# Optimization experiments

Hardware: AMD Instinct MI355X
Metric: run time of the kernel (lower is better)

The kernel has to match this reference:

```python
import math
import jax, jax.numpy as jnp
import numpy as np

B, T, C_IN, C_OUT, H, M = 16, 4096, 128, 64, 8, 30
TAU = 1.0
EPS = 1e-6


def _make_projection(m, d, seed=0):
    # FAVOR+ projection: stacked rows of transposed QR orthogonal blocks,
    # scaled by norms of gaussian rows (scaling=0 in the torch source).
    rng = np.random.RandomState(seed)
    blocks = []
    rows = 0
    while rows < m:
        q, _ = np.linalg.qr(rng.randn(d, d))
        blocks.append(q.T)
        rows += d
    final = np.vstack(blocks)[:m]
    multiplier = np.linalg.norm(rng.randn(m, d), axis=1)
    return jnp.asarray((multiplier[:, None] * final).astype(np.float32))


def _kernel_transform(data, proj, is_query):
    # softmax_kernel_transformation from the torch source
    d = data.shape[-1]
    data = data * (float(d) ** -0.25)
    ratio = 1.0 / math.sqrt(proj.shape[0])
    dd = jnp.einsum('bnhd,md->bnhm', data, proj)      # [B,T,H,M]
    diag = jnp.sum(data * data, axis=-1, keepdims=True) / 2.0
    if is_query:
        mx = jnp.max(dd, axis=-1, keepdims=True)
    else:
        mx = jnp.max(dd, axis=(1, 3), keepdims=True)  # max over features and seq
    return ratio * (jnp.exp(dd - diag - mx) + EPS)


def setup_inputs() -> dict:
    key = jax.random.key(0)
    ks = jax.random.split(key, 8)
    s_in = 1.0 / math.sqrt(C_IN)
    s_hid = 1.0 / math.sqrt(C_OUT * H)
    return {
        'x': jax.random.normal(ks[0], (B, T, C_IN), jnp.float32),
        'wq_w': jax.random.uniform(ks[1], (C_OUT * H, C_IN), jnp.float32, -s_in, s_in),
        'wq_b': jnp.zeros((C_OUT * H,), jnp.float32),
        'wk_w': jax.random.uniform(ks[2], (C_OUT * H, C_IN), jnp.float32, -s_in, s_in),
        'wk_b': jnp.zeros((C_OUT * H,), jnp.float32),
        'wv_w': jax.random.uniform(ks[3], (C_OUT * H, C_IN), jnp.float32, -s_in, s_in),
        'wv_b': jnp.zeros((C_OUT * H,), jnp.float32),
        'wo_w': jax.random.uniform(ks[4], (C_OUT, C_OUT * H), jnp.float32, -s_hid, s_hid),
        'wo_b': jnp.zeros((C_OUT,), jnp.float32),
        'proj': _make_projection(M, C_OUT, seed=0),
    }


def reference(x, wq_w, wq_b, wk_w, wk_b, wv_w, wv_b, wo_w, wo_b, proj):
    b, t, _ = x.shape
    inv_sqrt_tau = 1.0 / math.sqrt(TAU)
    q = (x @ wq_w.T + wq_b).reshape(b, t, H, C_OUT) * inv_sqrt_tau
    k = (x @ wk_w.T + wk_b).reshape(b, t, H, C_OUT) * inv_sqrt_tau
    v = (x @ wv_w.T + wv_b).reshape(b, t, H, C_OUT)
    q = _kernel_transform(q, proj, True)   # [B,T,H,M]
    k = _kernel_transform(k, proj, False)  # [B,T,H,M]
    # linear attention: O(T) kv state accumulation
    kvs = jnp.einsum('bnhm,bnhd->bhmd', k, v)
    num = jnp.einsum('bnhm,bhmd->bnhd', q, kvs)
    den = jnp.einsum('bnhm,bhm->bnh', q, jnp.sum(k, axis=1))
    out = num / den[..., None]             # [B,T,H,D]
    return out.reshape(b, t, H * C_OUT) @ wo_w.T + wo_b
```

## Files before the change

kernel.cpp:

```cpp
#include <hip/hip_runtime.h>
#include <cstdint>

typedef __attribute__((ext_vector_type(4))) float f32x4;
typedef __attribute__((ext_vector_type(8))) short short8;
typedef __attribute__((ext_vector_type(8))) unsigned short us8;

#define DEV __device__ __forceinline__

DEV unsigned short f2b(float f) {
  unsigned u = __builtin_bit_cast(unsigned, f);
  return (unsigned short)((u + 0x7fffu + ((u >> 16) & 1u)) >> 16);
}
DEV float b2f(unsigned short h) {
  unsigned u = ((unsigned)h) << 16;
  return __builtin_bit_cast(float, u);
}

constexpr float SQ_SCALE = 0.35355339059327379f;
constexpr float RATIO    = 0.18257418583505536f;
constexpr float REPS     = 0.18257418583505536e-6f;

constexpr size_t OF_WQKV  = 0;
constexpr size_t OF_WBP   = 262144;
constexpr size_t OF_XBF   = 270336;
constexpr size_t OF_XBFT  = 17047552;
constexpr size_t OF_PHIKT = 33824768;
constexpr size_t OF_S2    = 67379200;
constexpr size_t OF_KSUM  = 84156416;
constexpr size_t OF_GT    = 84172800;
constexpr size_t WS_NEED  = 84697088;

__global__ __launch_bounds__(256) void k_prep(
    const float* __restrict__ x, const float* __restrict__ wq,
    const float* __restrict__ wk, const float* __restrict__ bq,
    const float* __restrict__ bk, const float* __restrict__ proj,
    unsigned short* __restrict__ xbf, unsigned short* __restrict__ xbfT,
    unsigned short* __restrict__ wqkv, float* __restrict__ wbp) {
  int tid = threadIdx.x;
  if (blockIdx.x < 1024) {
    __shared__ unsigned short xt[128 * 72];
    int n0 = blockIdx.x * 64;
    int tok = tid & 63, cgrp = tid >> 6;
    const float* src = x + (size_t)(n0 + tok) * 128 + cgrp * 32;
    unsigned short* dst = xbf + (size_t)(n0 + tok) * 128 + cgrp * 32;
#pragma unroll
    for (int q8 = 0; q8 < 4; ++q8) {
      f32x4 a = *reinterpret_cast<const f32x4*>(src + q8 * 8);
      f32x4 c4 = *reinterpret_cast<const f32x4*>(src + q8 * 8 + 4);
      us8 o;
      o[0] = f2b(a[0]); o[1] = f2b(a[1]); o[2] = f2b(a[2]); o[3] = f2b(a[3]);
      o[4] = f2b(c4[0]); o[5] = f2b(c4[1]); o[6] = f2b(c4[2]); o[7] = f2b(c4[3]);
      *reinterpret_cast<us8*>(dst + q8 * 8) = o;
#pragma unroll
      for (int e = 0; e < 8; ++e) {
        int c = cgrp * 32 + q8 * 8 + e;
        *reinterpret_cast<unsigned short*>(((char*)xt) + c * 144 + tok * 2) = o[e];
      }
    }
    __syncthreads();
    int c2 = tid >> 1, half = tid & 1;
    size_t tbase = (size_t)blockIdx.x * 8192;
#pragma unroll
    for (int i = 0; i < 4; ++i) {
      us8 o = *reinterpret_cast<const us8*>(((const char*)xt) + c2 * 144 + half * 64 + i * 16);
      *reinterpret_cast<us8*>(xbfT + tbase + (size_t)tid * 32 + i * 8) = o;
    }
    return;
  }
  int bid = blockIdx.x - 1024;
  if (bid < 256) {
    int id = bid * 256 + tid;
    wqkv[id] = f2b(wk[id] * SQ_SCALE);
  } else if (bid < 272) {
    __shared__ float wsm[64 * 128];
    __shared__ float ps[32 * 64];
    __shared__ float bs[64];
    int db = bid - 256, mat2 = db >> 3, h = db & 7;
    const float* wsrc = (mat2 == 0) ? wq : wk;
    const float* bsrc = (mat2 == 0) ? bq : bk;
    for (int i = tid; i < 8192; i += 256) wsm[i] = wsrc[h * 8192 + i] * SQ_SCALE;
    for (int i = tid; i < 2048; i += 256) {
      int m = i >> 6, d = i & 63;
      ps[i] = (m < 30) ? proj[m * 64 + d] : 0.0f;
    }
    if (tid < 64) bs[tid] = bsrc[h * 64 + tid] * SQ_SCALE;
    __syncthreads();
    int m = tid >> 3, kseg = tid & 7;
    int col = 512 + mat2 * 256 + h * 32 + m;
#pragma unroll 4
    for (int kk = 0; kk < 16; ++kk) {
      int k = kseg * 16 + kk;
      float a = 0.f;
      for (int d = 0; d < 64; ++d) a += ps[m * 64 + d] * wsm[d * 128 + k];
      wqkv[col * 128 + k] = f2b(a);
    }
    if (tid < 32) {
      float a = 0.f;
      for (int d = 0; d < 64; ++d) a += ps[tid * 64 + d] * bs[d];
      wbp[512 + mat2 * 256 + h * 32 + tid] = a;
    }
  } else {
    for (int i = tid; i < 512; i += 256) wbp[i] = bk[i] * SQ_SCALE;
  }
}

DEV void stage_x(const unsigned short* xbf, unsigned short* xs, int n0, int tid) {
  int row = tid >> 2, seg = tid & 3;
  const unsigned short* src = xbf + (size_t)(n0 + row) * 128 + seg * 32;
#pragma unroll
  for (int q8 = 0; q8 < 4; ++q8) {
    us8 o = *reinterpret_cast<const us8*>(src + q8 * 8);
    int byte = (row * 256 + seg * 64 + q8 * 16) ^ ((row & 7) << 4);
    *reinterpret_cast<us8*>(((char*)xs) + byte) = o;
  }
}

__global__ __launch_bounds__(256) void k_qkv(
    const unsigned short* __restrict__ xbf, const unsigned short* __restrict__ wqkv,
    const float* __restrict__ wbp, unsigned short* __restrict__ phikT) {
  __shared__ unsigned short xs[64 * 128];
  __shared__ unsigned short scratch[4][2304];
  __shared__ float diag_s[512];

  int tid = threadIdx.x;
  int w = tid >> 6, l = tid & 63;
  int g = l >> 4, li = l & 15;
  int n0 = blockIdx.x * 64;

  stage_x(xbf, xs, n0, tid);
  __syncthreads();

  const short* wq_s = reinterpret_cast<const short*>(wqkv);
  char* scr = (char*)scratch[w];

  for (int j = 0; j < 3; ++j) {
    if (j == 2) __syncthreads();
    int bcol = (j < 2) ? (j * 256 + w * 64) : (768 + w * 64);

    f32x4 acc[4][4] = {};
#pragma unroll
    for (int ks = 0; ks < 4; ++ks) {
      short8 a[4], bb[4];
#pragma unroll
      for (int fi = 0; fi < 4; ++fi) {
        int tokl = fi * 16 + li;
        int byte = (tokl * 256 + (ks * 32 + g * 8) * 2) ^ ((tokl & 7) << 4);
        a[fi] = *reinterpret_cast<const short8*>(((const char*)xs) + byte);
      }
#pragma unroll
      for (int fj = 0; fj < 4; ++fj)
        bb[fj] = *reinterpret_cast<const short8*>(wq_s + (bcol + fj * 16 + li) * 128 + ks * 32 + g * 8);
#pragma unroll
      for (int fi = 0; fi < 4; ++fi)
#pragma unroll
        for (int fj = 0; fj < 4; ++fj)
          acc[fi][fj] = __builtin_amdgcn_mfma_f32_16x16x32_bf16(a[fi], bb[fj], acc[fi][fj], 0, 0, 0);
    }
#pragma unroll
    for (int fj = 0; fj < 4; ++fj) {
      float bias = wbp[bcol + fj * 16 + li];
#pragma unroll
      for (int fi = 0; fi < 4; ++fi)
#pragma unroll
        for (int r = 0; r < 4; ++r) acc[fi][fj][r] += bias;
    }

    if (j < 2) {
      int h = j * 4 + w;
      float t4[4][4];
#pragma unroll
      for (int fi = 0; fi < 4; ++fi)
#pragma unroll
        for (int r = 0; r < 4; ++r) {
          float s = 0.f;
#pragma unroll
          for (int fj = 0; fj < 4; ++fj) { float v = acc[fi][fj][r]; s += v * v; }
          t4[fi][r] = s;
        }
#pragma unroll
      for (int mask = 1; mask <= 8; mask <<= 1)
#pragma unroll
        for (int fi = 0; fi < 4; ++fi)
#pragma unroll
          for (int r = 0; r < 4; ++r)
            t4[fi][r] += __shfl_xor(t4[fi][r], mask, 64);
      if (li == 0) {
#pragma unroll
        for (int fi = 0; fi < 4; ++fi)
#pragma unroll
          for (int r = 0; r < 4; ++r)
            diag_s[h * 64 + fi * 16 + g * 4 + r] = 0.5f * t4[fi][r];
      }
    } else {
#pragma unroll
      for (int hp = 0; hp < 2; ++hp) {
        int h = w * 2 + hp;
#pragma unroll
        for (int fj2 = 0; fj2 < 2; ++fj2) {
          int m = fj2 * 16 + li;
          bool valid = (m < 30);
#pragma unroll
          for (int fi = 0; fi < 4; ++fi)
#pragma unroll
            for (int r = 0; r < 4; ++r) {
              int tok = fi * 16 + g * 4 + r;
              float ph = valid
                  ? (RATIO * __expf(acc[fi][hp * 2 + fj2][r] - diag_s[h * 64 + tok]) + REPS)
                  : 0.0f;
              *reinterpret_cast<unsigned short*>(scr + m * 144 + tok * 2) = f2b(ph);
            }
        }
        size_t gbase = (size_t)(h * 1024 + blockIdx.x) * 2048;
#pragma unroll
        for (int i = 0; i < 4; ++i) {
          us8 o = *reinterpret_cast<const us8*>(scr + (l >> 1) * 144 + (l & 1) * 64 + i * 16);
          *reinterpret_cast<us8*>(&phikT[gbase + (size_t)l * 32 + i * 8]) = o;
        }
      }
    }
  }
}

__global__ __launch_bounds__(256) void k_S(
    const unsigned short* __restrict__ phikT, const unsigned short* __restrict__ xbfT,
    float* __restrict__ S2, float* __restrict__ ksum) {
  int tid = threadIdx.x;
  int w = tid >> 6, l = tid & 63, g = l >> 4, li = l & 15;
  int bid = blockIdx.x;
  int bh = bid >> 3, chunk = bid & 7;
  int b = bh >> 3, h = bh & 7;
  int tb = b * 64 + chunk * 8;

  const short* pk = reinterpret_cast<const short*>(phikT);
  const short* xt = reinterpret_cast<const short*>(xbfT);

  float s0 = 0.f, s1 = 0.f;
  f32x4 acc[2][2] = {};
#pragma unroll 2
  for (int tile = 0; tile < 8; ++tile) {
    size_t abase = (size_t)(h * 1024 + tb + tile) * 2048;
    size_t bbase = (size_t)(tb + tile) * 8192 + (size_t)(w * 32) * 64;
#pragma unroll
    for (int ks = 0; ks < 2; ++ks) {
      int t = ks * 32 + g * 8;
      short8 a0 = *reinterpret_cast<const short8*>(pk + abase + li * 64 + t);
      short8 a1 = *reinterpret_cast<const short8*>(pk + abase + (16 + li) * 64 + t);
#pragma unroll
      for (int e = 0; e < 8; ++e) {
        s0 += b2f((unsigned short)a0[e]);
        s1 += b2f((unsigned short)a1[e]);
      }
      short8 b0 = *reinterpret_cast<const short8*>(xt + bbase + li * 64 + t);
      short8 b1 = *reinterpret_cast<const short8*>(xt + bbase + (16 + li) * 64 + t);
      acc[0][0] = __builtin_amdgcn_mfma_f32_16x16x32_bf16(a0, b0, acc[0][0], 0, 0, 0);
      acc[1][0] = __builtin_amdgcn_mfma_f32_16x16x32_bf16(a1, b0, acc[1][0], 0, 0, 0);
      acc[0][1] = __builtin_amdgcn_mfma_f32_16x16x32_bf16(a0, b1, acc[0][1], 0, 0, 0);
      acc[1][1] = __builtin_amdgcn_mfma_f32_16x16x32_bf16(a1, b1, acc[1][1], 0, 0, 0);
    }
  }
#pragma unroll
  for (int fm = 0; fm < 2; ++fm)
#pragma unroll
    for (int fc = 0; fc < 2; ++fc)
#pragma unroll
      for (int r = 0; r < 4; ++r) {
        int m = fm * 16 + g * 4 + r;
        int c = w * 32 + fc * 16 + li;
        S2[(size_t)bid * 4096 + m * 128 + c] = acc[fm][fc][r];
      }
  s0 += __shfl_xor(s0, 16, 64); s0 += __shfl_xor(s0, 32, 64);
  s1 += __shfl_xor(s1, 16, 64); s1 += __shfl_xor(s1, 32, 64);
  if (w == 0 && l < 16) {
    atomicAdd(&ksum[bh * 32 + l], s0);
    atomicAdd(&ksum[bh * 32 + 16 + l], s1);
  }
}

__global__ __launch_bounds__(256) void k_fold(
    const float* __restrict__ S2, const float* __restrict__ wv,
    const float* __restrict__ bv, const float* __restrict__ wo,
    const float* __restrict__ ksum, unsigned short* __restrict__ Gt) {
  __shared__ float ss[32 * 128];
  __shared__ float wvs[64 * 128];
  __shared__ float kvl[32 * 64];
  __shared__ float wos[64 * 64];
  __shared__ float bvs[64];
  __shared__ float kss[32];
  int tid = threadIdx.x;
  int bh = blockIdx.x, h = bh & 7;
  for (int i = tid; i < 4096; i += 256) {
    float a = 0.f;
#pragma unroll
    for (int c = 0; c < 8; ++c) a += S2[(size_t)(bh * 8 + c) * 4096 + i];
    ss[i] = a;
  }
  for (int i = tid; i < 8192; i += 256) wvs[i] = wv[(size_t)h * 8192 + i];
  {
    int c = tid >> 2, dseg = tid & 3;
#pragma unroll
    for (int jj = 0; jj < 16; ++jj) {
      int d = dseg * 16 + jj;
      wos[d * 64 + c] = wo[c * 512 + h * 64 + d];
    }
  }
  if (tid < 64) bvs[tid] = bv[h * 64 + tid];
  if (tid < 32) kss[tid] = ksum[bh * 32 + tid];
  __syncthreads();
  {
    int m = tid >> 3, dg = tid & 7;
#pragma unroll
    for (int i = 0; i < 8; ++i) {
      int d = dg * 8 + i;
      float a = kss[m] * bvs[d];
      for (int c = 0; c < 128; ++c) a += ss[m * 128 + c] * wvs[d * 128 + c];
      kvl[m * 64 + d] = a;
    }
  }
  __syncthreads();
  int cp = tid & 63, mseg = tid >> 6;
  us8 outv;
#pragma unroll
  for (int jj = 0; jj < 8; ++jj) {
    int m = mseg * 8 + jj;
    float a = 0.f;
    for (int d = 0; d < 64; ++d) a += kvl[m * 64 + d] * wos[d * 64 + cp];
    outv[jj] = f2b(a);
  }
  *reinterpret_cast<us8*>(Gt + ((size_t)bh * 64 + cp) * 32 + mseg * 8) = outv;
}

__global__ __launch_bounds__(256) void k_out(
    const unsigned short* __restrict__ xbf, const unsigned short* __restrict__ wqkv,
    const float* __restrict__ wbp, const unsigned short* __restrict__ Gt,
    const float* __restrict__ ksum, const float* __restrict__ wob,
    float* __restrict__ out) {
  __shared__ unsigned short phiqs[8 * 2048];

  int tid = threadIdx.x;
  int w = tid >> 6, l = tid & 63;
  int g = l >> 4, li = l & 15;
  int n0 = blockIdx.x * 64;
  int b = n0 >> 12;

  unsigned short* xs = phiqs;
  stage_x(xbf, xs, n0, tid);
  __syncthreads();

  const short* wq_s = reinterpret_cast<const short*>(wqkv);

  int bcol = 512 + w * 64;
  f32x4 acc[4][4] = {};
#pragma unroll
  for (int ks = 0; ks < 4; ++ks) {
    short8 a[4], bb[4];
#pragma unroll
    for (int fi = 0; fi < 4; ++fi) {
      int tokl = fi * 16 + li;
      int byte = (tokl * 256 + (ks * 32 + g * 8) * 2) ^ ((tokl & 7) << 4);
      a[fi] = *reinterpret_cast<const short8*>(((const char*)xs) + byte);
    }
#pragma unroll
    for (int fj = 0; fj < 4; ++fj)
      bb[fj] = *reinterpret_cast<const short8*>(wq_s + (bcol + fj * 16 + li) * 128 + ks * 32 + g * 8);
#pragma unroll
    for (int fi = 0; fi < 4; ++fi)
#pragma unroll
      for (int fj = 0; fj < 4; ++fj)
        acc[fi][fj] = __builtin_amdgcn_mfma_f32_16x16x32_bf16(a[fi], bb[fj], acc[fi][fj], 0, 0, 0);
  }
#pragma unroll
  for (int fj = 0; fj < 4; ++fj) {
    float bias = wbp[bcol + fj * 16 + li];
#pragma unroll
    for (int fi = 0; fi < 4; ++fi)
#pragma unroll
      for (int r = 0; r < 4; ++r) acc[fi][fj][r] += bias;
  }
  __syncthreads();

#pragma unroll
  for (int hp = 0; hp < 2; ++hp) {
    int h = w * 2 + hp;
    char* st = ((char*)phiqs) + h * 4096;
#pragma unroll
    for (int fj2 = 0; fj2 < 2; ++fj2) {
      int m = fj2 * 16 + li;
      bool valid = (m < 30);
#pragma unroll
      for (int fi = 0; fi < 4; ++fi)
#pragma unroll
        for (int r = 0; r < 4; ++r) {
          int tok = fi * 16 + g * 4 + r;
          float ph = valid ? __expf(acc[fi][hp * 2 + fj2][r]) : 0.0f;
          int byte = (tok * 64 + m * 2) ^ ((tok & 7) << 4);
          *reinterpret_cast<unsigned short*>(st + byte) = f2b(ph);
        }
    }
  }
  __syncthreads();

  const short* gt_s = reinterpret_cast<const short*>(Gt);
  int tokl = w * 16 + li;
  f32x4 oacc[4] = {};
#pragma unroll
  for (int h = 0; h < 8; ++h) {
    int bh = b * 8 + h;
    int abyte = h * 4096 + ((tokl * 64 + g * 16) ^ ((tokl & 7) << 4));
    short8 a = *reinterpret_cast<const short8*>(((const char*)phiqs) + abyte);
    const float* ksrow = ksum + bh * 32 + g * 8;
    float den = 0.f;
#pragma unroll
    for (int jj = 0; jj < 8; ++jj) den += b2f((unsigned short)a[jj]) * ksrow[jj];
    den += __shfl_xor(den, 16, 64);
    den += __shfl_xor(den, 32, 64);
    float rd = 1.0f / den;
    f32x4 nm[4];
#pragma unroll
    for (int fj = 0; fj < 4; ++fj) {
      short8 bb = *reinterpret_cast<const short8*>(gt_s + ((size_t)bh * 64 + fj * 16 + li) * 32 + g * 8);
      f32x4 z = {};
      nm[fj] = __builtin_amdgcn_mfma_f32_16x16x32_bf16(a, bb, z, 0, 0, 0);
    }
#pragma unroll
    for (int r = 0; r < 4; ++r) {
      float rdr = __shfl(rd, g * 4 + r, 64);
#pragma unroll
      for (int fj = 0; fj < 4; ++fj) oacc[fj][r] += nm[fj][r] * rdr;
    }
  }
#pragma unroll
  for (int fj = 0; fj < 4; ++fj) {
    float bias = wob[fj * 16 + li];
#pragma unroll
    for (int r = 0; r < 4; ++r) {
      int n = n0 + w * 16 + g * 4 + r;
      out[(size_t)n * 64 + fj * 16 + li] = oacc[fj][r] + bias;
    }
  }
}

extern "C" void kernel_launch(void* const* d_in, const int* in_sizes, int n_in,
                              void* d_out, int out_size, void* d_ws, size_t ws_size,
                              hipStream_t stream) {
  const int expect[10] = {8388608, 65536, 512, 65536, 512, 65536, 512, 32768, 64, 1920};
  if (n_in != 10) return;
  for (int i = 0; i < 10; ++i) if (in_sizes[i] != expect[i]) return;
  if (out_size != 4194304) return;
  if (ws_size < WS_NEED) return;

  const float* x    = (const float*)d_in[0];
  const float* wq   = (const float*)d_in[1];
  const float* bq   = (const float*)d_in[2];
  const float* wk   = (const float*)d_in[3];
  const float* bk   = (const float*)d_in[4];
  const float* wv   = (const float*)d_in[5];
  const float* bv   = (const float*)d_in[6];
  const float* wo   = (const float*)d_in[7];
  const float* wob  = (const float*)d_in[8];
  const float* proj = (const float*)d_in[9];

  char* ws = (char*)d_ws;
  unsigned short* wqkv  = (unsigned short*)(ws + OF_WQKV);
  float*          wbp   = (float*)(ws + OF_WBP);
  unsigned short* xbf   = (unsigned short*)(ws + OF_XBF);
  unsigned short* xbfT  = (unsigned short*)(ws + OF_XBFT);
  unsigned short* phikT = (unsigned short*)(ws + OF_PHIKT);
  float*          S2    = (float*)(ws + OF_S2);
  float*          ksum  = (float*)(ws + OF_KSUM);
  unsigned short* Gt    = (unsigned short*)(ws + OF_GT);

  (void)hipMemsetAsync(ws + OF_KSUM, 0, 16384, stream);

  k_prep<<<1297, 256, 0, stream>>>(x, wq, wk, bq, bk, proj, xbf, xbfT, wqkv, wbp);
  k_qkv<<<1024, 256, 0, stream>>>(xbf, wqkv, wbp, phikT);
  k_S<<<1024, 256, 0, stream>>>(phikT, xbfT, S2, ksum);
  k_fold<<<128, 256, 0, stream>>>(S2, wv, bv, wo, ksum, Gt);
  k_out<<<1024, 256, 0, stream>>>(xbf, wqkv, wbp, Gt, ksum, wob, (float*)d_out);
}
```

Before: 158.3 us.

## Fuse key feature-map computation into KV-state accumulation kernel, dropping phikT buffer

Merges the separate k_qkv and k_S kernels into one k_ks kernel. Each block recomputes the K projection and its random-feature map per head in registers, stages phi(K) in shared memory, and feeds it straight into the KV-state MFMA accumulation. This removes the global write and re-read of the phikT intermediate and one kernel launch. In exchange, the K/diag projection GEMM is now split per head, so the x tile and weight rows are reloaded from global for every head instead of being staged once per token tile, and extra block barriers are added per tile.

```diff
diff --git a/kernel.cpp b/kernel.cpp
--- a/kernel.cpp
+++ b/kernel.cpp
@@ -24,11 +24,10 @@
 constexpr size_t OF_WBP   = 262144;
 constexpr size_t OF_XBF   = 270336;
 constexpr size_t OF_XBFT  = 17047552;
-constexpr size_t OF_PHIKT = 33824768;
-constexpr size_t OF_S2    = 67379200;
-constexpr size_t OF_KSUM  = 84156416;
-constexpr size_t OF_GT    = 84172800;
-constexpr size_t WS_NEED  = 84697088;
+constexpr size_t OF_S2    = 33824768;
+constexpr size_t OF_KSUM  = 50601984;
+constexpr size_t OF_GT    = 50618368;
+constexpr size_t WS_NEED  = 51142656;
 
 __global__ __launch_bounds__(256) void k_prep(
     const float* __restrict__ x, const float* __restrict__ wq,
@@ -58,8 +57,8 @@
       }
     }
     __syncthreads();
+    size_t tbase = (size_t)blockIdx.x * 8192;
     int c2 = tid >> 1, half = tid & 1;
-    size_t tbase = (size_t)blockIdx.x * 8192;
 #pragma unroll
     for (int i = 0; i < 4; ++i) {
       us8 o = *reinterpret_cast<const us8*>(((const char*)xt) + c2 * 144 + half * 64 + i * 16);
@@ -115,115 +114,12 @@
   }
 }
 
-__global__ __launch_bounds__(256) void k_qkv(
-    const unsigned short* __restrict__ xbf, const unsigned short* __restrict__ wqkv,
-    const float* __restrict__ wbp, unsigned short* __restrict__ phikT) {
-  __shared__ unsigned short xs[64 * 128];
-  __shared__ unsigned short scratch[4][2304];
-  __shared__ float diag_s[512];
-
-  int tid = threadIdx.x;
-  int w = tid >> 6, l = tid & 63;
-  int g = l >> 4, li = l & 15;
-  int n0 = blockIdx.x * 64;
-
-  stage_x(xbf, xs, n0, tid);
-  __syncthreads();
-
-  const short* wq_s = reinterpret_cast<const short*>(wqkv);
-  char* scr = (char*)scratch[w];
-
-  for (int j = 0; j < 3; ++j) {
-    if (j == 2) __syncthreads();
-    int bcol = (j < 2) ? (j * 256 + w * 64) : (768 + w * 64);
-
-    f32x4 acc[4][4] = {};
-#pragma unroll
-    for (int ks = 0; ks < 4; ++ks) {
-      short8 a[4], bb[4];
-#pragma unroll
-      for (int fi = 0; fi < 4; ++fi) {
-        int tokl = fi * 16 + li;
-        int byte = (tokl * 256 + (ks * 32 + g * 8) * 2) ^ ((tokl & 7) << 4);
-        a[fi] = *reinterpret_cast<const short8*>(((const char*)xs) + byte);
-      }
-#pragma unroll
-      for (int fj = 0; fj < 4; ++fj)
-        bb[fj] = *reinterpret_cast<const short8*>(wq_s + (bcol + fj * 16 + li) * 128 + ks * 32 + g * 8);
-#pragma unroll
-      for (int fi = 0; fi < 4; ++fi)
-#pragma unroll
-        for (int fj = 0; fj < 4; ++fj)
-          acc[fi][fj] = __builtin_amdgcn_mfma_f32_16x16x32_bf16(a[fi], bb[fj], acc[fi][fj], 0, 0, 0);
-    }
-#pragma unroll
-    for (int fj = 0; fj < 4; ++fj) {
-      float bias = wbp[bcol + fj * 16 + li];
-#pragma unroll
-      for (int fi = 0; fi < 4; ++fi)
-#pragma unroll
-        for (int r = 0; r < 4; ++r) acc[fi][fj][r] += bias;
-    }
-
-    if (j < 2) {
-      int h = j * 4 + w;
-      float t4[4][4];
-#pragma unroll
-      for (int fi = 0; fi < 4; ++fi)
-#pragma unroll
-        for (int r = 0; r < 4; ++r) {
-          float s = 0.f;
-#pragma unroll
-          for (int fj = 0; fj < 4; ++fj) { float v = acc[fi][fj][r]; s += v * v; }
-          t4[fi][r] = s;
-        }
-#pragma unroll
-      for (int mask = 1; mask <= 8; mask <<= 1)
-#pragma unroll
-        for (int fi = 0; fi < 4; ++fi)
-#pragma unroll
-          for (int r = 0; r < 4; ++r)
-            t4[fi][r] += __shfl_xor(t4[fi][r], mask, 64);
-      if (li == 0) {
-#pragma unroll
-        for (int fi = 0; fi < 4; ++fi)
-#pragma unroll
-          for (int r = 0; r < 4; ++r)
-            diag_s[h * 64 + fi * 16 + g * 4 + r] = 0.5f * t4[fi][r];
-      }
-    } else {
-#pragma unroll
-      for (int hp = 0; hp < 2; ++hp) {
-        int h = w * 2 + hp;
-#pragma unroll
-        for (int fj2 = 0; fj2 < 2; ++fj2) {
-          int m = fj2 * 16 + li;
-          bool valid = (m < 30);
-#pragma unroll
-          for (int fi = 0; fi < 4; ++fi)
-#pragma unroll
-            for (int r = 0; r < 4; ++r) {
-              int tok = fi * 16 + g * 4 + r;
-              float ph = valid
-                  ? (RATIO * __expf(acc[fi][hp * 2 + fj2][r] - diag_s[h * 64 + tok]) + REPS)
-                  : 0.0f;
-              *reinterpret_cast<unsigned short*>(scr + m * 144 + tok * 2) = f2b(ph);
-            }
-        }
-        size_t gbase = (size_t)(h * 1024 + blockIdx.x) * 2048;
-#pragma unroll
-        for (int i = 0; i < 4; ++i) {
-          us8 o = *reinterpret_cast<const us8*>(scr + (l >> 1) * 144 + (l & 1) * 64 + i * 16);
-          *reinterpret_cast<us8*>(&phikT[gbase + (size_t)l * 32 + i * 8]) = o;
-        }
-      }
-    }
-  }
-}
-
-__global__ __launch_bounds__(256) void k_S(
-    const unsigned short* __restrict__ phikT, const unsigned short* __restrict__ xbfT,
+__global__ __launch_bounds__(256) void k_ks(
+    const unsigned short* __restrict__ xbf, const unsigned short* __restrict__ xbfT,
+    const unsigned short* __restrict__ wqkv, const float* __restrict__ wbp,
     float* __restrict__ S2, float* __restrict__ ksum) {
+  __shared__ unsigned short phit[32 * 72];
+
   int tid = threadIdx.x;
   int w = tid >> 6, l = tid & 63, g = l >> 4, li = l & 15;
   int bid = blockIdx.x;
@@ -231,33 +127,95 @@
   int b = bh >> 3, h = bh & 7;
   int tb = b * 64 + chunk * 8;
 
-  const short* pk = reinterpret_cast<const short*>(phikT);
-  const short* xt = reinterpret_cast<const short*>(xbfT);
-
-  float s0 = 0.f, s1 = 0.f;
-  f32x4 acc[2][2] = {};
-#pragma unroll 2
+  const short* xb_s = reinterpret_cast<const short*>(xbf);
+  const short* xt_s = reinterpret_cast<const short*>(xbfT);
+  const short* wq_s = reinterpret_cast<const short*>(wqkv);
+
+  float biask[4], biasd[2];
+#pragma unroll
+  for (int fj = 0; fj < 4; ++fj) biask[fj] = wbp[h * 64 + fj * 16 + li];
+#pragma unroll
+  for (int fj = 0; fj < 2; ++fj) biasd[fj] = wbp[768 + h * 32 + fj * 16 + li];
+
+  float kpart[2] = {0, 0};
+  f32x4 sacc[2][2] = {};
+
   for (int tile = 0; tile < 8; ++tile) {
-    size_t abase = (size_t)(h * 1024 + tb + tile) * 2048;
+    int n0 = (tb + tile) * 64;
+    f32x4 acc[6] = {};
+#pragma unroll
+    for (int ks = 0; ks < 4; ++ks) {
+      short8 a = *reinterpret_cast<const short8*>(
+          xb_s + (size_t)(n0 + w * 16 + li) * 128 + ks * 32 + g * 8);
+      short8 bk4[4], bd2[2];
+#pragma unroll
+      for (int fj = 0; fj < 4; ++fj)
+        bk4[fj] = *reinterpret_cast<const short8*>(
+            wq_s + (size_t)(h * 64 + fj * 16 + li) * 128 + ks * 32 + g * 8);
+#pragma unroll
+      for (int fj = 0; fj < 2; ++fj)
+        bd2[fj] = *reinterpret_cast<const short8*>(
+            wq_s + (size_t)(768 + h * 32 + fj * 16 + li) * 128 + ks * 32 + g * 8);
+#pragma unroll
+      for (int fj = 0; fj < 4; ++fj)
+        acc[fj] = __builtin_amdgcn_mfma_f32_16x16x32_bf16(a, bk4[fj], acc[fj], 0, 0, 0);
+#pragma unroll
+      for (int fj = 0; fj < 2; ++fj)
+        acc[4 + fj] = __builtin_amdgcn_mfma_f32_16x16x32_bf16(a, bd2[fj], acc[4 + fj], 0, 0, 0);
+    }
+#pragma unroll
+    for (int fj = 0; fj < 4; ++fj)
+#pragma unroll
+      for (int r = 0; r < 4; ++r) acc[fj][r] += biask[fj];
+#pragma unroll
+    for (int fj = 0; fj < 2; ++fj)
+#pragma unroll
+      for (int r = 0; r < 4; ++r) acc[4 + fj][r] += biasd[fj];
+
+    float t4[4];
+#pragma unroll
+    for (int r = 0; r < 4; ++r) {
+      float s = 0.f;
+#pragma unroll
+      for (int fj = 0; fj < 4; ++fj) { float v = acc[fj][r]; s += v * v; }
+      t4[r] = s;
+    }
+#pragma unroll
+    for (int mask = 1; mask <= 8; mask <<= 1)
+#pragma unroll
+      for (int r = 0; r < 4; ++r) t4[r] += __shfl_xor(t4[r], mask, 64);
+
+#pragma unroll
+    for (int fj = 0; fj < 2; ++fj) {
+      int m = fj * 16 + li;
+      bool valid = (m < 30);
+#pragma unroll
+      for (int r = 0; r < 4; ++r) {
+        int tok = w * 16 + g * 4 + r;
+        float ph = valid ? (RATIO * __expf(acc[4 + fj][r] - 0.5f * t4[r]) + REPS) : 0.f;
+        unsigned short pb = f2b(ph);
+        kpart[fj] += b2f(pb);
+        *reinterpret_cast<unsigned short*>(((char*)phit) + m * 144 + tok * 2) = pb;
+      }
+    }
+    __syncthreads();
+
     size_t bbase = (size_t)(tb + tile) * 8192 + (size_t)(w * 32) * 64;
 #pragma unroll
     for (int ks = 0; ks < 2; ++ks) {
       int t = ks * 32 + g * 8;
-      short8 a0 = *reinterpret_cast<const short8*>(pk + abase + li * 64 + t);
-      short8 a1 = *reinterpret_cast<const short8*>(pk + abase + (16 + li) * 64 + t);
-#pragma unroll
-      for (int e = 0; e < 8; ++e) {
-        s0 += b2f((unsigned short)a0[e]);
-        s1 += b2f((unsigned short)a1[e]);
-      }
-      short8 b0 = *reinterpret_cast<const short8*>(xt + bbase + li * 64 + t);
-      short8 b1 = *reinterpret_cast<const short8*>(xt + bbase + (16 + li) * 64 + t);
-      acc[0][0] = __builtin_amdgcn_mfma_f32_16x16x32_bf16(a0, b0, acc[0][0], 0, 0, 0);
-      acc[1][0] = __builtin_amdgcn_mfma_f32_16x16x32_bf16(a1, b0, acc[1][0], 0, 0, 0);
-      acc[0][1] = __builtin_amdgcn_mfma_f32_16x16x32_bf16(a0, b1, acc[0][1], 0, 0, 0);
-      acc[1][1] = __builtin_amdgcn_mfma_f32_16x16x32_bf16(a1, b1, acc[1][1], 0, 0, 0);
-    }
-  }
+      short8 a0 = *reinterpret_cast<const short8*>(((const char*)phit) + li * 144 + t * 2);
+      short8 a1 = *reinterpret_cast<const short8*>(((const char*)phit) + (16 + li) * 144 + t * 2);
+      short8 b0 = *reinterpret_cast<const short8*>(xt_s + bbase + li * 64 + t);
+      short8 b1 = *reinterpret_cast<const short8*>(xt_s + bbase + (16 + li) * 64 + t);
+      sacc[0][0] = __builtin_amdgcn_mfma_f32_16x16x32_bf16(a0, b0, sacc[0][0], 0, 0, 0);
+      sacc[1][0] = __builtin_amdgcn_mfma_f32_16x16x32_bf16(a1, b0, sacc[1][0], 0, 0, 0);
+      sacc[0][1] = __builtin_amdgcn_mfma_f32_16x16x32_bf16(a0, b1, sacc[0][1], 0, 0, 0);
+      sacc[1][1] = __builtin_amdgcn_mfma_f32_16x16x32_bf16(a1, b1, sacc[1][1], 0, 0, 0);
+    }
+    __syncthreads();
+  }
+
 #pragma unroll
   for (int fm = 0; fm < 2; ++fm)
 #pragma unroll
@@ -266,13 +224,16 @@
       for (int r = 0; r < 4; ++r) {
         int m = fm * 16 + g * 4 + r;
         int c = w * 32 + fc * 16 + li;
-        S2[(size_t)bid * 4096 + m * 128 + c] = acc[fm][fc][r];
+        S2[(size_t)bid * 4096 + m * 128 + c] = sacc[fm][fc][r];
       }
-  s0 += __shfl_xor(s0, 16, 64); s0 += __shfl_xor(s0, 32, 64);
-  s1 += __shfl_xor(s1, 16, 64); s1 += __shfl_xor(s1, 32, 64);
-  if (w == 0 && l < 16) {
-    atomicAdd(&ksum[bh * 32 + l], s0);
-    atomicAdd(&ksum[bh * 32 + 16 + l], s1);
+#pragma unroll
+  for (int fj = 0; fj < 2; ++fj) {
+    kpart[fj] += __shfl_xor(kpart[fj], 16, 64);
+    kpart[fj] += __shfl_xor(kpart[fj], 32, 64);
+  }
+  if (l < 16) {
+    atomicAdd(&ksum[bh * 32 + l], kpart[0]);
+    atomicAdd(&ksum[bh * 32 + 16 + l], kpart[1]);
   }
 }
 
@@ -460,20 +421,18 @@
   const float* proj = (const float*)d_in[9];
 
   char* ws = (char*)d_ws;
-  unsigned short* wqkv  = (unsigned short*)(ws + OF_WQKV);
-  float*          wbp   = (float*)(ws + OF_WBP);
-  unsigned short* xbf   = (unsigned short*)(ws + OF_XBF);
-  unsigned short* xbfT  = (unsigned short*)(ws + OF_XBFT);
-  unsigned short* phikT = (unsigned short*)(ws + OF_PHIKT);
-  float*          S2    = (float*)(ws + OF_S2);
-  float*          ksum  = (float*)(ws + OF_KSUM);
-  unsigned short* Gt    = (unsigned short*)(ws + OF_GT);
+  unsigned short* wqkv = (unsigned short*)(ws + OF_WQKV);
+  float*          wbp  = (float*)(ws + OF_WBP);
+  unsigned short* xbf  = (unsigned short*)(ws + OF_XBF);
+  unsigned short* xbfT = (unsigned short*)(ws + OF_XBFT);
+  float*          S2   = (float*)(ws + OF_S2);
+  float*          ksum = (float*)(ws + OF_KSUM);
+  unsigned short* Gt   = (unsigned short*)(ws + OF_GT);
 
   (void)hipMemsetAsync(ws + OF_KSUM, 0, 16384, stream);
 
   k_prep<<<1297, 256, 0, stream>>>(x, wq, wk, bq, bk, proj, xbf, xbfT, wqkv, wbp);
-  k_qkv<<<1024, 256, 0, stream>>>(xbf, wqkv, wbp, phikT);
-  k_S<<<1024, 256, 0, stream>>>(phikT, xbfT, S2, ksum);
+  k_ks<<<1024, 256, 0, stream>>>(xbf, xbfT, wqkv, wbp, S2, ksum);
   k_fold<<<128, 256, 0, stream>>>(S2, wv, bv, wo, ksum, Gt);
   k_out<<<1024, 256, 0, stream>>>(xbf, wqkv, wbp, Gt, ksum, wob, (float*)d_out);
 }
```

New measurement: 142.0 us. -10.3%, faster.
